# Kernel optimization log

Hardware: AMD Instinct MI355X
Metric: run time of the kernel (lower is better)

Reference implementation:

```python
import jax, jax.numpy as jnp
import numpy as np

# Hyperparameters from init_kwargs (linear beta schedule, is_lin=True branch)
BETA_1 = 1e-4
BETA_T = 0.02
T = 1000
B = 8192
IMG = 32


def _schedule_coeffs():
    """Closed-form coefficients for the original's per-sample iterative loop.

    The original recursion (iterative_process) is, for iter = 0..t-1:
        x_{k+1} = x_k * s_k + normal * (beta_k^2 * I)
    where s_k = sqrt_alphas_bar[k] (NB: the original multiplies by the
    *cumulative* sqrt-alpha at every step, and the 'std' is beta^2 * eye(32)
    broadcast over channels). Unrolling gives
        x_t = x_0 * P_t + normal * I * C_t
    with P_t = prod_{k<t} s_k and C_t = sum_{k<t} beta_k^2 * prod_{k<j<t} s_j,
    which satisfy P_{t} = P_{t-1}*s_{t-1}, C_t = C_{t-1}*s_{t-1} + beta_{t-1}^2.
    """
    betas = jnp.linspace(BETA_1, BETA_T, T + 1, dtype=jnp.float32)
    alphas_cumprod = jnp.cumprod(1.0 - betas)
    s = jnp.sqrt(alphas_cumprod)          # sqrt_alphas_bar, shape (T+1,)
    P = jnp.cumprod(s)                    # P[k] = P_{t=k+1}

    def step(c, xs):
        s_k, b_k = xs
        c = c * s_k + b_k * b_k
        return c, c

    _, C = jax.lax.scan(step, jnp.float32(0.0), (s, betas))  # C[k] = C_{t=k+1}
    return P, C


def setup_inputs() -> dict:
    key = jax.random.key(0)
    k1, k2, k3 = jax.random.split(key, 3)
    x_0 = jax.random.uniform(k1, (B, 3, IMG, IMG), dtype=jnp.float32)
    normal = jax.random.normal(k2, (B, 3, IMG, IMG), dtype=jnp.float32)
    # original: torch.randint(low=1, high=T+1, size=(B,))
    timesteps = jax.random.randint(k3, (B,), 1, T + 1, dtype=jnp.int32)
    return {"x_0": x_0, "normal": normal, "timesteps": timesteps}


def reference(x_0, normal, timesteps):
    P, C = _schedule_coeffs()
    idx = timesteps - 1                   # t in [1, T] -> array index t-1
    Pt = P[idx][:, None, None, None]      # (B,1,1,1)
    Ct = C[idx][:, None, None, None]      # (B,1,1,1)
    eye = jnp.eye(IMG, dtype=x_0.dtype)   # diagonal mask from beta*eye(32)
    # x_t = x_0 * P_t + normal * (C_t * I), broadcast over (B,3,32,32)
    x_t = x_0 * Pt + normal * eye * Ct
    return x_t
```

## Files before the change

### kernel.cpp

```cpp
#include <hip/hip_runtime.h>


constexpr int T_STEPS = 1000;
constexpr int BATCH   = 8192;
constexpr int K1_BLOCKS  = BATCH * 3;
constexpr int N_DIAG     = BATCH * 3 * 32;
constexpr int K2_BLOCKS  = N_DIAG / 256;

struct Tables { float P[T_STEPS]; float C[T_STEPS]; };

constexpr double csqrt_d(double x) {
    if (x <= 0.0) return 0.0;
    double scale = 1.0;
    while (x < 0.25) { x *= 4.0;  scale *= 0.5; }
    while (x >= 1.0) { x *= 0.25; scale *= 2.0; }
    double g = 0.5 * (x + 1.0);
    for (int i = 0; i < 40; ++i) {
        double ng = 0.5 * (g + x / g);
        if (ng == g) break;
        g = ng;
    }
    return g * scale;
}

constexpr Tables make_tables() {
    Tables t{};
    const float beta1 = 1e-4f;
    const float betaT = 0.02f;
    const float delta = (betaT - beta1) / 1000.0f;
    float ac = 1.0f, P = 1.0f, c = 0.0f;
    for (int k = 0; k < T_STEPS; ++k) {
        float beta = beta1 + (float)k * delta;
        ac = ac * (1.0f - beta);
        float s = (float)csqrt_d((double)ac);
        P = P * s;
        c = c * s + beta * beta;
        t.P[k] = P;
        t.C[k] = c;
    }
    return t;
}

__device__ __constant__ Tables d_tbl = make_tables();

__global__ __launch_bounds__(256) void scale_kernel(
    const float* __restrict__ x0,
    const int*   __restrict__ tsteps,
    float*       __restrict__ out)
{
    const int bid = blockIdx.x;
    const int img = bid / 3;
    const int t   = tsteps[img] - 1;
    const float Pt = d_tbl.P[t];

    const int f = bid * 256 + threadIdx.x;
    const float4 x = reinterpret_cast<const float4*>(x0)[f];
    float4 r;
    r.x = x.x * Pt;
    r.y = x.y * Pt;
    r.z = x.z * Pt;
    r.w = x.w * Pt;
    reinterpret_cast<float4*>(out)[f] = r;
}

__global__ __launch_bounds__(256) void diag_kernel(
    const float* __restrict__ nrm,
    const int*   __restrict__ tsteps,
    float*       __restrict__ out)
{
    const int gid = blockIdx.x * 256 + threadIdx.x;
    const int img = gid / 96;
    const int rem = gid - img * 96;
    const int off = img * 3072 + rem * 32 + (rem & 31);

    const int t    = tsteps[img] - 1;
    const float Ct = d_tbl.C[t];

    out[off] = fmaf(nrm[off], Ct, out[off]);
}

extern "C" void kernel_launch(void* const* d_in, const int* in_sizes, int n_in,
                              void* d_out, int out_size, void* d_ws, size_t ws_size,
                              hipStream_t stream) {
    const float* x0     = (const float*)d_in[0];
    const float* nrm    = (const float*)d_in[1];
    const int*   tsteps = (const int*)d_in[2];
    float*       out    = (float*)d_out;

    scale_kernel<<<K1_BLOCKS, 256, 0, stream>>>(x0, tsteps, out);
    diag_kernel <<<K2_BLOCKS, 256, 0, stream>>>(nrm, tsteps, out);
}
```

Before: 256.0 us.

## Fuse scale and diagonal-noise kernels into one per-image pass

Replaces the two-kernel approach (a full scale pass followed by a scattered read-modify-write of diagonal elements) with a single kernel where each block handles one image. Each thread loads three float4s of x0, scales them by P_t, and adds C_t times the noise only at diagonal positions, reading just the needed noise elements. This removes the second pass over the output and one kernel launch. The cost is fewer, larger blocks and some divergent sparse loads.

```diff
diff --git a/kernel.cpp b/kernel.cpp
--- a/kernel.cpp
+++ b/kernel.cpp
@@ -3,9 +3,7 @@
 
 constexpr int T_STEPS = 1000;
 constexpr int BATCH   = 8192;
-constexpr int K1_BLOCKS  = BATCH * 3;
-constexpr int N_DIAG     = BATCH * 3 * 32;
-constexpr int K2_BLOCKS  = N_DIAG / 256;
+constexpr int BLOCKS  = BATCH;
 
 struct Tables { float P[T_STEPS]; float C[T_STEPS]; };
 
@@ -43,40 +41,56 @@
 
 __device__ __constant__ Tables d_tbl = make_tables();
 
-__global__ __launch_bounds__(256) void scale_kernel(
+__global__ __launch_bounds__(256) void gd_fused_kernel(
     const float* __restrict__ x0,
-    const int*   __restrict__ tsteps,
-    float*       __restrict__ out)
-{
-    const int bid = blockIdx.x;
-    const int img = bid / 3;
-    const int t   = tsteps[img] - 1;
-    const float Pt = d_tbl.P[t];
-
-    const int f = bid * 256 + threadIdx.x;
-    const float4 x = reinterpret_cast<const float4*>(x0)[f];
-    float4 r;
-    r.x = x.x * Pt;
-    r.y = x.y * Pt;
-    r.z = x.z * Pt;
-    r.w = x.w * Pt;
-    reinterpret_cast<float4*>(out)[f] = r;
-}
-
-__global__ __launch_bounds__(256) void diag_kernel(
     const float* __restrict__ nrm,
     const int*   __restrict__ tsteps,
     float*       __restrict__ out)
 {
-    const int gid = blockIdx.x * 256 + threadIdx.x;
-    const int img = gid / 96;
-    const int rem = gid - img * 96;
-    const int off = img * 3072 + rem * 32 + (rem & 31);
-
-    const int t    = tsteps[img] - 1;
+    const int img = blockIdx.x;
+    const int t   = __builtin_amdgcn_readfirstlane(tsteps[img] - 1);
+    const float Pt = d_tbl.P[t];
     const float Ct = d_tbl.C[t];
 
-    out[off] = fmaf(nrm[off], Ct, out[off]);
+    const int tid = threadIdx.x;
+    const int h  = tid >> 3;
+    const int w0 = (tid & 7) << 2;
+    const int d  = h - w0;
+    const bool has_diag = (unsigned)d < 4u;
+
+    const int f0 = img * 768 + tid;
+    const float4* __restrict__ x4 = reinterpret_cast<const float4*>(x0);
+    float4*       __restrict__ o4 = reinterpret_cast<float4*>(out);
+
+    const float4 xa = x4[f0];
+    const float4 xb = x4[f0 + 256];
+    const float4 xc = x4[f0 + 512];
+
+    float na = 0.0f, nb = 0.0f, nc = 0.0f;
+    if (has_diag) {
+        na = nrm[((f0      ) << 2) + d];
+        nb = nrm[((f0 + 256) << 2) + d];
+        nc = nrm[((f0 + 512) << 2) + d];
+    }
+
+    float4 r;
+    r.x = xa.x * Pt + (d == 0 ? na * Ct : 0.0f);
+    r.y = xa.y * Pt + (d == 1 ? na * Ct : 0.0f);
+    r.z = xa.z * Pt + (d == 2 ? na * Ct : 0.0f);
+    r.w = xa.w * Pt + (d == 3 ? na * Ct : 0.0f);
+    o4[f0] = r;
+
+    r.x = xb.x * Pt + (d == 0 ? nb * Ct : 0.0f);
+    r.y = xb.y * Pt + (d == 1 ? nb * Ct : 0.0f);
+    r.z = xb.z * Pt + (d == 2 ? nb * Ct : 0.0f);
+    r.w = xb.w * Pt + (d == 3 ? nb * Ct : 0.0f);
+    o4[f0 + 256] = r;
+
+    r.x = xc.x * Pt + (d == 0 ? nc * Ct : 0.0f);
+    r.y = xc.y * Pt + (d == 1 ? nc * Ct : 0.0f);
+    r.z = xc.z * Pt + (d == 2 ? nc * Ct : 0.0f);
+    r.w = xc.w * Pt + (d == 3 ? nc * Ct : 0.0f);
+    o4[f0 + 512] = r;
 }
 
 extern "C" void kernel_launch(void* const* d_in, const int* in_sizes, int n_in,
@@ -87,6 +101,5 @@
     const int*   tsteps = (const int*)d_in[2];
     float*       out    = (float*)d_out;
 
-    scale_kernel<<<K1_BLOCKS, 256, 0, stream>>>(x0, tsteps, out);
-    diag_kernel <<<K2_BLOCKS, 256, 0, stream>>>(nrm, tsteps, out);
+    gd_fused_kernel<<<BLOCKS, 256, 0, stream>>>(x0, nrm, tsteps, out);
 }
```

New measurement: 242.4 us. 1.06x faster.
